# Kernel optimization log

Measured on AMD Instinct MI355X. Metric: run time of the kernel, lower is better.

Reference implementation:

```python
import jax, jax.numpy as jnp
import numpy as np

EMBED_DIM = 1024
NUM_HEADS = 16
HEAD_DIM = EMBED_DIM // NUM_HEADS
ROPE_BASE = 10000.0


def rotate_half(x):
    # interleaved variant: pairs (x0,x1) -> (-x1, x0)
    x1 = x[..., ::2]
    x2 = x[..., 1::2]
    return jnp.stack((-x2, x1), axis=-1).reshape(x.shape)


def rope_tables(T, dim, dtype):
    inv_freq = 1.0 / (ROPE_BASE ** (jnp.arange(0, dim, 2, dtype=jnp.float32) / dim))
    t = jnp.arange(T, dtype=jnp.float32)
    freqs = t[:, None] * inv_freq[None, :]          # [T, dim/2]
    emb = jnp.concatenate((freqs, freqs), axis=-1)  # [T, dim]
    return jnp.cos(emb).astype(dtype), jnp.sin(emb).astype(dtype)


def setup_inputs() -> dict:
    key = jax.random.key(0)
    kx, kq, ko = jax.random.split(key, 3)
    B, T, D = 2, 2048, EMBED_DIM
    x = jax.random.normal(kx, (B, T, D), dtype=jnp.float32)
    s = 1.0 / np.sqrt(D)
    Wqkv = jax.random.normal(kq, (D, 3 * D), dtype=jnp.float32) * s
    Wout = jax.random.normal(ko, (D, D), dtype=jnp.float32) * s
    return {"x": x, "Wqkv": Wqkv, "Wout": Wout}


def reference(x, Wqkv, Wout):
    B, T, D = x.shape
    H, hd = NUM_HEADS, HEAD_DIM
    qkv = x @ Wqkv                                   # [B,T,3D]
    q, k, v = jnp.split(qkv, 3, axis=-1)
    q = q.reshape(B, T, H, hd).transpose(0, 2, 1, 3)  # [B,H,T,hd]
    k = k.reshape(B, T, H, hd).transpose(0, 2, 1, 3)
    v = v.reshape(B, T, H, hd).transpose(0, 2, 1, 3)
    cos, sin = rope_tables(T, hd, x.dtype)           # [T,hd]
    cos = cos[None, None, :, :]
    sin = sin[None, None, :, :]
    q = q * cos + rotate_half(q) * sin
    k = k * cos + rotate_half(k) * sin
    scale = 1.0 / np.sqrt(hd).astype(np.float32)
    attn = jnp.einsum('bhtd,bhsd->bhts', q, k) * scale  # [B,H,T,T]
    attn = jax.nn.softmax(attn, axis=-1)
    out = jnp.einsum('bhts,bhsd->bhtd', attn, v)     # [B,H,T,hd]
    out = out.transpose(0, 2, 1, 3).reshape(B, T, D)
    return out @ Wout
```

## Files before the change

### kernel.cpp

```cpp
#include <hip/hip_runtime.h>
#include <hip/hip_bf16.h>
#include <stdint.h>


typedef unsigned short u16;
typedef short bf16x8 __attribute__((ext_vector_type(8)));
typedef float f32x4  __attribute__((ext_vector_type(4)));

#if defined(__has_builtin) && __has_builtin(__builtin_amdgcn_exp2f)
#define EXP2F(x) __builtin_amdgcn_exp2f(x)
#else
#define EXP2F(x) exp2f(x)
#endif

__device__ __forceinline__ u16 f2b(float f) {
  uint32_t u = __float_as_uint(f);
  u += 0x7fffu + ((u >> 16) & 1u);
  return (u16)(u >> 16);
}
__device__ __forceinline__ uint32_t pk2(float a, float b) {
  return (uint32_t)f2b(a) | ((uint32_t)f2b(b) << 16);
}
__device__ __forceinline__ uint32_t pkbf(float a, float b) {
  __hip_bfloat162 h = __float22bfloat162_rn(make_float2(a, b));
  union { __hip_bfloat162 h2; uint32_t u; } cv; cv.h2 = h;
  return cv.u;
}

__device__ __forceinline__ void gl2lds16(const void* g, void* l) {
  __builtin_amdgcn_global_load_lds(
      (const __attribute__((address_space(1))) unsigned int*)g,
      (__attribute__((address_space(3))) unsigned int*)l, 16, 0, 0);
}

__global__ void sniff_kernel(const u16* x, int* flag) {
  __shared__ int cnt;
  if (threadIdx.x == 0) cnt = 0;
  __syncthreads();
  int c = 0;
  for (int i = threadIdx.x; i < 4096; i += 256) {
    float a = fabsf(__uint_as_float(((uint32_t)x[2*i]) << 16));
    if (a > 1e-3f && a < 100.f) c++;
  }
  atomicAdd(&cnt, c);
  __syncthreads();
  if (threadIdx.x == 0) *flag = (cnt > 2048) ? 1 : 0;
}

__global__ __launch_bounds__(256) void convert_x_kernel(
    const void* __restrict__ xv, const int* __restrict__ flag, u16* __restrict__ Xb)
{
  const int isb = *flag;
  const size_t i = ((size_t)blockIdx.x * 256 + threadIdx.x) * 8;
  if (isb) {
    *(uint4*)&Xb[i] = *(const uint4*)((const u16*)xv + i);
  } else {
    const float* s = (const float*)xv + i;
    float4 a = *(const float4*)s, b = *(const float4*)(s + 4);
    uint4 p;
    p.x = pk2(a.x, a.y); p.y = pk2(a.z, a.w);
    p.z = pk2(b.x, b.y); p.w = pk2(b.z, b.w);
    *(uint4*)&Xb[i] = p;
  }
}

__global__ __launch_bounds__(256) void transpose_w_kernel(
    const void* __restrict__ src, u16* __restrict__ dst,
    int K, int N, const int* __restrict__ flag)
{
  __shared__ u16 Lt[64 * 72];
  const int isb = *flag;
  const int tid = threadIdx.x;
  const int n0 = blockIdx.x * 64, k0 = blockIdx.y * 64;
  const int r = tid >> 2, cseg = (tid & 3) << 4;
  u16 t[16];
  if (isb) {
    const u16* s = (const u16*)src + (size_t)(k0 + r) * N + n0 + cseg;
    *(uint4*)&t[0] = *(const uint4*)s;
    *(uint4*)&t[8] = *(const uint4*)(s + 8);
  } else {
    const float* s = (const float*)src + (size_t)(k0 + r) * N + n0 + cseg;
    #pragma unroll
    for (int j = 0; j < 4; j++) {
      float4 v = *(const float4*)(s + j * 4);
      t[j*4+0] = f2b(v.x); t[j*4+1] = f2b(v.y); t[j*4+2] = f2b(v.z); t[j*4+3] = f2b(v.w);
    }
  }
  #pragma unroll
  for (int j = 0; j < 16; j++) Lt[(cseg + j) * 72 + r] = t[j];
  __syncthreads();
  const int n = tid >> 2, kseg = (tid & 3) << 4;
  uint4 u0 = *(const uint4*)&Lt[n * 72 + kseg];
  uint4 u1 = *(const uint4*)&Lt[n * 72 + kseg + 8];
  u16* d = dst + (size_t)(n0 + n) * K + k0 + kseg;
  *(uint4*)d = u0;
  *(uint4*)(d + 8) = u1;
}

__global__ __launch_bounds__(256) void rope_table_kernel(float2* __restrict__ CS) {
  const int idx = blockIdx.x * 256 + threadIdx.x;
  const int t = idx >> 5, f = idx & 31;
  float invf = __expf(-(float)f * 0.2878231366242557f);
  float th = (float)t * invf;
  float sn, cs;
  sincosf(th, &sn, &cs);
  CS[idx] = make_float2(cs, sn);
}

__global__ __launch_bounds__(256) void qkv_kernel(
    const u16* __restrict__ Xb, const u16* __restrict__ Wt,
    const float2* __restrict__ CS,
    u16* __restrict__ Q, u16* __restrict__ K, u16* __restrict__ Vt)
{
  __shared__ u16 As[128 * 64];
  __shared__ u16 Bs[128 * 64];
  const int tid = threadIdx.x;
  const int n0 = blockIdx.x * 128;
  const int m0 = blockIdx.y * 128;
  const int w = tid >> 6, l = tid & 63, lr = l & 15, lq = l >> 4;
  const int mrow0 = (w & 1) * 64;
  const int ncol0 = (w >> 1) * 64;
  const int srow = tid >> 3;
  const int gseg = (tid & 7) ^ (srow & 7);

  f32x4 acc[4][4] = {};

  for (int k0 = 0; k0 < 1024; k0 += 64) {
    __syncthreads();
    #pragma unroll
    for (int rd = 0; rd < 4; rd++) {
      const int row = srow + rd * 32;
      gl2lds16(Xb + (size_t)(m0 + row) * 1024 + k0 + gseg * 8, &As[tid * 8 + rd * 2048]);
      gl2lds16(Wt + (size_t)(n0 + row) * 1024 + k0 + gseg * 8, &Bs[tid * 8 + rd * 2048]);
    }
    __syncthreads();
    #pragma unroll
    for (int kc = 0; kc < 2; kc++) {
      bf16x8 af[4], bf[4];
      #pragma unroll
      for (int i = 0; i < 4; i++) {
        const int seg = ((kc << 2) | lq) ^ (lr & 7);
        af[i] = *(const bf16x8*)&As[(mrow0 + i * 16 + lr) * 64 + seg * 8];
        bf[i] = *(const bf16x8*)&Bs[(ncol0 + i * 16 + lr) * 64 + seg * 8];
      }
      #pragma unroll
      for (int mb = 0; mb < 4; mb++)
        #pragma unroll
        for (int nb = 0; nb < 4; nb++)
          acc[mb][nb] = __builtin_amdgcn_mfma_f32_16x16x32_bf16(af[mb], bf[nb], acc[mb][nb], 0, 0, 0);
    }
  }

  const int col0 = n0 + ncol0;
  const int sec = col0 >> 10;
  const int h = (col0 >> 6) & 15;
  if (sec == 2) {
    #pragma unroll
    for (int mb = 0; mb < 4; mb++) {
      const int row0 = m0 + mrow0 + mb * 16 + lq * 4;
      const int b = row0 >> 11, t0 = row0 & 2047;
      #pragma unroll
      for (int nb = 0; nb < 4; nb++) {
        const int d = nb * 16 + lr;
        uint2 uv;
        uv.x = pk2(acc[mb][nb][0], acc[mb][nb][1]);
        uv.y = pk2(acc[mb][nb][2], acc[mb][nb][3]);
        *(uint2*)&Vt[(((size_t)b * 16 + h) * 64 + d) * 2048 + t0] = uv;
      }
    }
  } else {
    u16* dst = (sec == 0) ? Q : K;
    const float qscale = 0.125f * 1.44269504f;
    #pragma unroll
    for (int mb = 0; mb < 4; mb++) {
      const int row0 = m0 + mrow0 + mb * 16 + lq * 4;
      const int b = row0 >> 11, t0 = row0 & 2047;
      #pragma unroll
      for (int nb = 0; nb < 4; nb++) {
        const int d = nb * 16 + lr;
        const int f = d & 31;
        #pragma unroll
        for (int r = 0; r < 4; r++) {
          const int t = t0 + r;
          float2 cs = CS[t * 32 + f];
          float val = acc[mb][nb][r];
          float prt = __shfl_xor(val, 1, 64);
          float res = fmaf(val, cs.x, ((d & 1) ? prt : -prt) * cs.y);
          if (sec == 0) res *= qscale;
          dst[(((size_t)b * 16 + h) * 2048 + t) * 64 + d] = f2b(res);
        }
      }
    }
  }
}

__global__ __launch_bounds__(256, 3) void attn_kernel(
    const u16* __restrict__ Q, const u16* __restrict__ K,
    const u16* __restrict__ Vt, u16* __restrict__ ATT,
    float* __restrict__ Op, float* __restrict__ Ls)
{
  __shared__ u16 Ks[2][64 * 64];
  __shared__ u16 Vs[2][64 * 64];
  __shared__ u16 Ps[4][32 * 72];
  const int tid = threadIdx.x;
  const int w = tid >> 6, l = tid & 63, lr = l & 15, lq = l >> 4;
  const int bh = blockIdx.x >> 4;
  const int qt = blockIdx.x & 15;
  const int ns = gridDim.y, sh = blockIdx.y;
  const int slen = 2048 / ns;
  const int sbeg = sh * slen;
  const size_t base = (size_t)bh * (2048 * 64);
  const int qrow0 = qt * 128 + w * 32;
  u16* Psw = &Ps[w][0];

  bf16x8 qf[2][2];
  #pragma unroll
  for (int mb = 0; mb < 2; mb++)
    #pragma unroll
    for (int kc = 0; kc < 2; kc++)
      qf[mb][kc] = *(const bf16x8*)(Q + base + (size_t)(qrow0 + mb * 16 + lr) * 64 + kc * 32 + lq * 8);

  f32x4 oa[4][2] = {};
  float lsum[2] = {0.f, 0.f};

  const int srow = tid >> 3;

  auto stage = [&](int buf, int s0) {
    #pragma unroll
    for (int rd = 0; rd < 2; rd++) {
      const int row = srow + rd * 32;
      const int gs = (tid & 7) ^ (row & 7);
      gl2lds16(K + base + (size_t)(s0 + row) * 64 + gs * 8, &Ks[buf][tid * 8 + rd * 2048]);
      gl2lds16(Vt + base + (size_t)row * 2048 + s0 + gs * 8, &Vs[buf][tid * 8 + rd * 2048]);
    }
  };

  stage(0, sbeg);
  const int nt = slen >> 6;

  #pragma unroll 1
  for (int t = 0; t < nt; t++) {
    const int buf = t & 1;
    __syncthreads();
    if (t + 1 < nt) stage(buf ^ 1, sbeg + (t + 1) * 64);

    bf16x8 kf[4][2], vf[4][2];
    #pragma unroll
    for (int nb = 0; nb < 4; nb++)
      #pragma unroll
      for (int kc = 0; kc < 2; kc++) {
        const int seg = ((kc << 2) | lq) ^ (lr & 7);
        kf[nb][kc] = *(const bf16x8*)&Ks[buf][(nb * 16 + lr) * 64 + seg * 8];
        vf[nb][kc] = *(const bf16x8*)&Vs[buf][(nb * 16 + lr) * 64 + seg * 8];
      }

    #pragma unroll
    for (int sb = 0; sb < 4; sb++) {
      #pragma unroll
      for (int mb = 0; mb < 2; mb++) {
        f32x4 st = {};
        st = __builtin_amdgcn_mfma_f32_16x16x32_bf16(kf[sb][0], qf[mb][0], st, 0, 0, 0);
        st = __builtin_amdgcn_mfma_f32_16x16x32_bf16(kf[sb][1], qf[mb][1], st, 0, 0, 0);
        float e0 = EXP2F(st[0]), e1 = EXP2F(st[1]), e2 = EXP2F(st[2]), e3 = EXP2F(st[3]);
        lsum[mb] += (e0 + e1) + (e2 + e3);
        uint2 pp;
        pp.x = pkbf(e0, e1);
        pp.y = pkbf(e2, e3);
        *(uint2*)&Psw[(mb * 16 + lr) * 72 + sb * 16 + lq * 4] = pp;
      }
    }

    #pragma unroll
    for (int mb = 0; mb < 2; mb++) {
      bf16x8 pf0 = *(const bf16x8*)&Psw[(mb * 16 + lr) * 72 + lq * 8];
      bf16x8 pf1 = *(const bf16x8*)&Psw[(mb * 16 + lr) * 72 + 32 + lq * 8];
      #pragma unroll
      for (int db = 0; db < 4; db++) {
        oa[db][mb] = __builtin_amdgcn_mfma_f32_16x16x32_bf16(vf[db][0], pf0, oa[db][mb], 0, 0, 0);
        oa[db][mb] = __builtin_amdgcn_mfma_f32_16x16x32_bf16(vf[db][1], pf1, oa[db][mb], 0, 0, 0);
      }
    }
  }

  #pragma unroll
  for (int mb = 0; mb < 2; mb++) {
    float v = lsum[mb];
    v += __shfl_xor(v, 16, 64);
    v += __shfl_xor(v, 32, 64);
    lsum[mb] = v;
  }

  const int b = bh >> 4, h = bh & 15;
  if (ns == 1) {
    #pragma unroll
    for (int mb = 0; mb < 2; mb++) {
      const float inv = 1.f / lsum[mb];
      const int t = qrow0 + mb * 16 + lr;
      u16* dst = ATT + ((size_t)(b * 2048 + t)) * 1024 + h * 64;
      #pragma unroll
      for (int db = 0; db < 4; db++) {
        uint2 u;
        u.x = pkbf(oa[db][mb][0] * inv, oa[db][mb][1] * inv);
        u.y = pkbf(oa[db][mb][2] * inv, oa[db][mb][3] * inv);
        *(uint2*)&dst[db * 16 + lq * 4] = u;
      }
    }
  } else {
    float* op = Op + (size_t)sh * (65536ull * 64);
    #pragma unroll
    for (int mb = 0; mb < 2; mb++) {
      const size_t row = (size_t)bh * 2048 + qrow0 + mb * 16 + lr;
      #pragma unroll
      for (int db = 0; db < 4; db++)
        *(f32x4*)&op[row * 64 + db * 16 + lq * 4] = oa[db][mb];
      if (lq == 0) Ls[(size_t)sh * 65536 + row] = lsum[mb];
    }
  }
}

__global__ __launch_bounds__(256) void combine_kernel(
    const float* __restrict__ Op, const float* __restrict__ Ls, u16* __restrict__ ATT)
{
  const int idx = blockIdx.x * 256 + threadIdx.x;
  const int R = idx >> 3;
  const int c = (idx & 7) * 8;
  const float* p0 = Op + (size_t)R * 64 + c;
  const float* p1 = p0 + 65536ull * 64;
  f32x4 a0 = *(const f32x4*)p0, a1 = *(const f32x4*)(p0 + 4);
  f32x4 b0 = *(const f32x4*)p1, b1 = *(const f32x4*)(p1 + 4);
  const float inv = 1.f / (Ls[R] + Ls[65536 + R]);
  const int bh = R >> 11, trow = R & 2047;
  const int b = bh >> 4, h = bh & 15;
  u16* d = ATT + ((size_t)(b * 2048 + trow)) * 1024 + h * 64 + c;
  uint4 u;
  u.x = pkbf((a0[0] + b0[0]) * inv, (a0[1] + b0[1]) * inv);
  u.y = pkbf((a0[2] + b0[2]) * inv, (a0[3] + b0[3]) * inv);
  u.z = pkbf((a1[0] + b1[0]) * inv, (a1[1] + b1[1]) * inv);
  u.w = pkbf((a1[2] + b1[2]) * inv, (a1[3] + b1[3]) * inv);
  *(uint4*)d = u;
}

__global__ __launch_bounds__(256) void outproj_kernel(
    const u16* __restrict__ A, const u16* __restrict__ Wt,
    const int* __restrict__ flag, void* __restrict__ outv)
{
  __shared__ u16 As[128 * 64];
  __shared__ u16 Bs[128 * 64];
  const int isb = *flag;
  const int tid = threadIdx.x;
  const int n0 = blockIdx.x * 128;
  const int m0 = blockIdx.y * 128;
  const int w = tid >> 6, l = tid & 63, lr = l & 15, lq = l >> 4;
  const int mrow0 = (w & 1) * 64;
  const int ncol0 = (w >> 1) * 64;
  const int srow = tid >> 3;
  const int gseg = (tid & 7) ^ (srow & 7);

  f32x4 acc[4][4] = {};

  for (int k0 = 0; k0 < 1024; k0 += 64) {
    __syncthreads();
    #pragma unroll
    for (int rd = 0; rd < 4; rd++) {
      const int row = srow + rd * 32;
      gl2lds16(A + (size_t)(m0 + row) * 1024 + k0 + gseg * 8, &As[tid * 8 + rd * 2048]);
      gl2lds16(Wt + (size_t)(n0 + row) * 1024 + k0 + gseg * 8, &Bs[tid * 8 + rd * 2048]);
    }
    __syncthreads();
    #pragma unroll
    for (int kc = 0; kc < 2; kc++) {
      bf16x8 af[4], bf[4];
      #pragma unroll
      for (int i = 0; i < 4; i++) {
        const int seg = ((kc << 2) | lq) ^ (lr & 7);
        af[i] = *(const bf16x8*)&As[(mrow0 + i * 16 + lr) * 64 + seg * 8];
        bf[i] = *(const bf16x8*)&Bs[(ncol0 + i * 16 + lr) * 64 + seg * 8];
      }
      #pragma unroll
      for (int mb = 0; mb < 4; mb++)
        #pragma unroll
        for (int nb = 0; nb < 4; nb++)
          acc[mb][nb] = __builtin_amdgcn_mfma_f32_16x16x32_bf16(af[mb], bf[nb], acc[mb][nb], 0, 0, 0);
    }
  }
  #pragma unroll
  for (int mb = 0; mb < 4; mb++) {
    const int row = m0 + mrow0 + mb * 16 + lq * 4;
    #pragma unroll
    for (int nb = 0; nb < 4; nb++) {
      const int col = n0 + ncol0 + nb * 16 + lr;
      #pragma unroll
      for (int r = 0; r < 4; r++) {
        float val = acc[mb][nb][r];
        if (isb) ((u16*)outv)[(size_t)(row + r) * 1024 + col] = f2b(val);
        else     ((float*)outv)[(size_t)(row + r) * 1024 + col] = val;
      }
    }
  }
}

extern "C" void kernel_launch(void* const* d_in, const int* in_sizes, int n_in,
                              void* d_out, int out_size, void* d_ws, size_t ws_size,
                              hipStream_t stream)
{
  const void* x    = d_in[0];
  const void* wqkv = d_in[1];
  const void* wout = d_in[2];
  char* ws = (char*)d_ws;
  const size_t MB = 1024 * 1024;
  int*    flag   = (int*)ws;
  float2* CS     = (float2*)(ws + 1024);
  u16*    Xb     = (u16*)(ws + 1 * MB);
  u16*    ATT    = Xb;
  u16*    Wqkvt  = (u16*)(ws + 9 * MB);
  u16*    Woutt  = (u16*)(ws + 15 * MB);
  u16*    Q      = (u16*)(ws + 17 * MB);
  u16*    K      = (u16*)(ws + 25 * MB);
  u16*    Vt     = (u16*)(ws + 33 * MB);
  float*  Op     = (float*)(ws + 41 * MB);
  float*  Ls     = (float*)(ws + 75 * MB);

  const bool split = ws_size >= 76 * MB;
  const int ns = split ? 2 : 1;

  sniff_kernel<<<1, 256, 0, stream>>>((const u16*)x, flag);
  convert_x_kernel<<<2048, 256, 0, stream>>>(x, flag, Xb);
  transpose_w_kernel<<<dim3(48, 16), 256, 0, stream>>>(wqkv, Wqkvt, 1024, 3072, flag);
  transpose_w_kernel<<<dim3(16, 16), 256, 0, stream>>>(wout, Woutt, 1024, 1024, flag);
  rope_table_kernel<<<256, 256, 0, stream>>>(CS);
  qkv_kernel<<<dim3(24, 32), 256, 0, stream>>>(Xb, Wqkvt, CS, Q, K, Vt);
  attn_kernel<<<dim3(512, ns), 256, 0, stream>>>(Q, K, Vt, ATT, Op, Ls);
  if (split)
    combine_kernel<<<2048, 256, 0, stream>>>(Op, Ls, ATT);
  outproj_kernel<<<dim3(8, 32), 256, 0, stream>>>(ATT, Woutt, flag, d_out);
}
```

Before: 226.8 us.

## Fuse prep kernels and double attention query tile per block

Merges the x conversion, both weight transposes and the RoPE table build into one prep kernel to cut launch overhead. The attention kernel now handles 64 query rows per wave (256 per block), so each staged K/V tile is reused across twice as many queries, with half the grid and occupancy bound lowered to 2. The P scratch buffer moves to an XOR-swizzled 64-wide layout to avoid LDS bank conflicts, and some bf16 packing switches to the hardware conversion intrinsic. Risks include higher register pressure, lower occupancy, and fewer blocks to fill the GPU.

Result: faster. 214.6 us (-5.4%).

```diff
diff --git a/kernel.cpp b/kernel.cpp
--- a/kernel.cpp
+++ b/kernel.cpp
@@ -47,31 +47,9 @@
   if (threadIdx.x == 0) *flag = (cnt > 2048) ? 1 : 0;
 }
 
-__global__ __launch_bounds__(256) void convert_x_kernel(
-    const void* __restrict__ xv, const int* __restrict__ flag, u16* __restrict__ Xb)
-{
-  const int isb = *flag;
-  const size_t i = ((size_t)blockIdx.x * 256 + threadIdx.x) * 8;
-  if (isb) {
-    *(uint4*)&Xb[i] = *(const uint4*)((const u16*)xv + i);
-  } else {
-    const float* s = (const float*)xv + i;
-    float4 a = *(const float4*)s, b = *(const float4*)(s + 4);
-    uint4 p;
-    p.x = pk2(a.x, a.y); p.y = pk2(a.z, a.w);
-    p.z = pk2(b.x, b.y); p.w = pk2(b.z, b.w);
-    *(uint4*)&Xb[i] = p;
-  }
-}
-
-__global__ __launch_bounds__(256) void transpose_w_kernel(
-    const void* __restrict__ src, u16* __restrict__ dst,
-    int K, int N, const int* __restrict__ flag)
-{
-  __shared__ u16 Lt[64 * 72];
-  const int isb = *flag;
-  const int tid = threadIdx.x;
-  const int n0 = blockIdx.x * 64, k0 = blockIdx.y * 64;
+__device__ __forceinline__ void tr_tile(const void* src, u16* dst, int Kd, int N,
+                                        int n0, int k0, int isb, u16* Lt, int tid)
+{
   const int r = tid >> 2, cseg = (tid & 3) << 4;
   u16 t[16];
   if (isb) {
@@ -92,19 +70,47 @@
   const int n = tid >> 2, kseg = (tid & 3) << 4;
   uint4 u0 = *(const uint4*)&Lt[n * 72 + kseg];
   uint4 u1 = *(const uint4*)&Lt[n * 72 + kseg + 8];
-  u16* d = dst + (size_t)(n0 + n) * K + k0 + kseg;
+  u16* d = dst + (size_t)(n0 + n) * Kd + k0 + kseg;
   *(uint4*)d = u0;
   *(uint4*)(d + 8) = u1;
 }
 
-__global__ __launch_bounds__(256) void rope_table_kernel(float2* __restrict__ CS) {
-  const int idx = blockIdx.x * 256 + threadIdx.x;
-  const int t = idx >> 5, f = idx & 31;
-  float invf = __expf(-(float)f * 0.2878231366242557f);
-  float th = (float)t * invf;
-  float sn, cs;
-  sincosf(th, &sn, &cs);
-  CS[idx] = make_float2(cs, sn);
+__global__ __launch_bounds__(256) void prep_kernel(
+    const void* __restrict__ x, const void* __restrict__ wqkv,
+    const void* __restrict__ wout, const int* __restrict__ flag,
+    u16* __restrict__ Xb, u16* __restrict__ Wqkvt, u16* __restrict__ Woutt,
+    float2* __restrict__ CS)
+{
+  __shared__ u16 Lt[64 * 72];
+  const int isb = *flag;
+  const int bid = blockIdx.x, tid = threadIdx.x;
+  if (bid < 2048) {
+    const size_t i = ((size_t)bid * 256 + tid) * 8;
+    if (isb) {
+      *(uint4*)&Xb[i] = *(const uint4*)((const u16*)x + i);
+    } else {
+      const float* s = (const float*)x + i;
+      float4 a = *(const float4*)s, b = *(const float4*)(s + 4);
+      uint4 p;
+      p.x = pkbf(a.x, a.y); p.y = pkbf(a.z, a.w);
+      p.z = pkbf(b.x, b.y); p.w = pkbf(b.z, b.w);
+      *(uint4*)&Xb[i] = p;
+    }
+  } else if (bid < 2816) {
+    const int b = bid - 2048;
+    tr_tile(wqkv, Wqkvt, 1024, 3072, (b % 48) * 64, (b / 48) * 64, isb, Lt, tid);
+  } else if (bid < 3072) {
+    const int b = bid - 2816;
+    tr_tile(wout, Woutt, 1024, 1024, (b % 16) * 64, (b / 16) * 64, isb, Lt, tid);
+  } else {
+    const int idx = (bid - 3072) * 256 + tid;
+    const int t = idx >> 5, f = idx & 31;
+    float invf = __expf(-(float)f * 0.2878231366242557f);
+    float th = (float)t * invf;
+    float sn, cs;
+    sincosf(th, &sn, &cs);
+    CS[idx] = make_float2(cs, sn);
+  }
 }
 
 __global__ __launch_bounds__(256) void qkv_kernel(
@@ -163,8 +169,8 @@
       for (int nb = 0; nb < 4; nb++) {
         const int d = nb * 16 + lr;
         uint2 uv;
-        uv.x = pk2(acc[mb][nb][0], acc[mb][nb][1]);
-        uv.y = pk2(acc[mb][nb][2], acc[mb][nb][3]);
+        uv.x = pkbf(acc[mb][nb][0], acc[mb][nb][1]);
+        uv.y = pkbf(acc[mb][nb][2], acc[mb][nb][3]);
         *(uint2*)&Vt[(((size_t)b * 16 + h) * 64 + d) * 2048 + t0] = uv;
       }
     }
@@ -194,34 +200,34 @@
   }
 }
 
-__global__ __launch_bounds__(256, 3) void attn_kernel(
+__global__ __launch_bounds__(256, 2) void attn_kernel(
     const u16* __restrict__ Q, const u16* __restrict__ K,
     const u16* __restrict__ Vt, u16* __restrict__ ATT,
     float* __restrict__ Op, float* __restrict__ Ls)
 {
   __shared__ u16 Ks[2][64 * 64];
   __shared__ u16 Vs[2][64 * 64];
-  __shared__ u16 Ps[4][32 * 72];
+  __shared__ u16 Ps[4][64 * 64];
   const int tid = threadIdx.x;
   const int w = tid >> 6, l = tid & 63, lr = l & 15, lq = l >> 4;
-  const int bh = blockIdx.x >> 4;
-  const int qt = blockIdx.x & 15;
+  const int bh = blockIdx.x >> 3;
+  const int qt = blockIdx.x & 7;
   const int ns = gridDim.y, sh = blockIdx.y;
   const int slen = 2048 / ns;
   const int sbeg = sh * slen;
   const size_t base = (size_t)bh * (2048 * 64);
-  const int qrow0 = qt * 128 + w * 32;
+  const int qrow0 = qt * 256 + w * 64;
   u16* Psw = &Ps[w][0];
 
-  bf16x8 qf[2][2];
+  bf16x8 qf[4][2];
   #pragma unroll
-  for (int mb = 0; mb < 2; mb++)
+  for (int mb = 0; mb < 4; mb++)
     #pragma unroll
     for (int kc = 0; kc < 2; kc++)
       qf[mb][kc] = *(const bf16x8*)(Q + base + (size_t)(qrow0 + mb * 16 + lr) * 64 + kc * 32 + lq * 8);
 
-  f32x4 oa[4][2] = {};
-  float lsum[2] = {0.f, 0.f};
+  f32x4 oa[4][4] = {};
+  float lsum[4] = {0.f, 0.f, 0.f, 0.f};
 
   const int srow = tid >> 3;
 
@@ -257,7 +263,7 @@
     #pragma unroll
     for (int sb = 0; sb < 4; sb++) {
       #pragma unroll
-      for (int mb = 0; mb < 2; mb++) {
+      for (int mb = 0; mb < 4; mb++) {
         f32x4 st = {};
         st = __builtin_amdgcn_mfma_f32_16x16x32_bf16(kf[sb][0], qf[mb][0], st, 0, 0, 0);
         st = __builtin_amdgcn_mfma_f32_16x16x32_bf16(kf[sb][1], qf[mb][1], st, 0, 0, 0);
@@ -266,14 +272,17 @@
         uint2 pp;
         pp.x = pkbf(e0, e1);
         pp.y = pkbf(e2, e3);
-        *(uint2*)&Psw[(mb * 16 + lr) * 72 + sb * 16 + lq * 4] = pp;
-      }
-    }
-
-    #pragma unroll
-    for (int mb = 0; mb < 2; mb++) {
-      bf16x8 pf0 = *(const bf16x8*)&Psw[(mb * 16 + lr) * 72 + lq * 8];
-      bf16x8 pf1 = *(const bf16x8*)&Psw[(mb * 16 + lr) * 72 + 32 + lq * 8];
+        const int pseg = ((sb << 1) | (lq >> 1)) ^ (lr & 7);
+        *(uint2*)&Psw[(mb * 16 + lr) * 64 + pseg * 8 + (lq & 1) * 4] = pp;
+      }
+    }
+
+    #pragma unroll
+    for (int mb = 0; mb < 4; mb++) {
+      const int rs0 = lq ^ (lr & 7);
+      const int rs1 = (4 | lq) ^ (lr & 7);
+      bf16x8 pf0 = *(const bf16x8*)&Psw[(mb * 16 + lr) * 64 + rs0 * 8];
+      bf16x8 pf1 = *(const bf16x8*)&Psw[(mb * 16 + lr) * 64 + rs1 * 8];
       #pragma unroll
       for (int db = 0; db < 4; db++) {
         oa[db][mb] = __builtin_amdgcn_mfma_f32_16x16x32_bf16(vf[db][0], pf0, oa[db][mb], 0, 0, 0);
@@ -283,7 +292,7 @@
   }
 
   #pragma unroll
-  for (int mb = 0; mb < 2; mb++) {
+  for (int mb = 0; mb < 4; mb++) {
     float v = lsum[mb];
     v += __shfl_xor(v, 16, 64);
     v += __shfl_xor(v, 32, 64);
@@ -293,7 +302,7 @@
   const int b = bh >> 4, h = bh & 15;
   if (ns == 1) {
     #pragma unroll
-    for (int mb = 0; mb < 2; mb++) {
+    for (int mb = 0; mb < 4; mb++) {
       const float inv = 1.f / lsum[mb];
       const int t = qrow0 + mb * 16 + lr;
       u16* dst = ATT + ((size_t)(b * 2048 + t)) * 1024 + h * 64;
@@ -308,7 +317,7 @@
   } else {
     float* op = Op + (size_t)sh * (65536ull * 64);
     #pragma unroll
-    for (int mb = 0; mb < 2; mb++) {
+    for (int mb = 0; mb < 4; mb++) {
       const size_t row = (size_t)bh * 2048 + qrow0 + mb * 16 + lr;
       #pragma unroll
       for (int db = 0; db < 4; db++)
@@ -424,12 +433,9 @@
   const int ns = split ? 2 : 1;
 
   sniff_kernel<<<1, 256, 0, stream>>>((const u16*)x, flag);
-  convert_x_kernel<<<2048, 256, 0, stream>>>(x, flag, Xb);
-  transpose_w_kernel<<<dim3(48, 16), 256, 0, stream>>>(wqkv, Wqkvt, 1024, 3072, flag);
-  transpose_w_kernel<<<dim3(16, 16), 256, 0, stream>>>(wout, Woutt, 1024, 1024, flag);
-  rope_table_kernel<<<256, 256, 0, stream>>>(CS);
+  prep_kernel<<<3328, 256, 0, stream>>>(x, wqkv, wout, flag, Xb, Wqkvt, Woutt, CS);
   qkv_kernel<<<dim3(24, 32), 256, 0, stream>>>(Xb, Wqkvt, CS, Q, K, Vt);
-  attn_kernel<<<dim3(512, ns), 256, 0, stream>>>(Q, K, Vt, ATT, Op, Ls);
+  attn_kernel<<<dim3(256, ns), 256, 0, stream>>>(Q, K, Vt, ATT, Op, Ls);
   if (split)
     combine_kernel<<<2048, 256, 0, stream>>>(Op, Ls, ATT);
   outproj_kernel<<<dim3(8, 32), 256, 0, stream>>>(ATT, Woutt, flag, d_out);
```
